# Kernel tuning notes

Hardware: AMD Instinct MI355X
Metric: run time of the kernel (lower is better)

## Reference

```python
import jax, jax.numpy as jnp
import numpy as np

ALPHA = 0.2  # LeakyReLU negative slope
NEG_INF = -9e15  # matches torch's -9e15 mask value


def gat_head(h, mask, W, a):
    # h: [N, Fin], W: [Fin, Fout], a: [2*Fout]
    # Faithful to torch GraphAttentionLayer but WITHOUT materializing the
    # N x N x 2F pairwise concat: a^T [Wh_i ; Wh_j] = (Wh_i . a1) + (Wh_j . a2).
    Wh = h @ W                                  # [N, F]
    F = W.shape[1]
    f = Wh @ a[:F]                              # [N] source term
    g = Wh @ a[F:]                              # [N] target term
    e = jax.nn.leaky_relu(f[:, None] + g[None, :], ALPHA)  # [N, N]
    e = jnp.where(mask, e, NEG_INF)
    attn = jax.nn.softmax(e, axis=1)            # row-wise softmax over neighbors
    return jax.nn.elu(attn @ Wh)                # [N, F]


def multi_head_gat(x, mask, W_heads, a_heads, W_out, a_out):
    # W_heads: [H, Fin, F], a_heads: [H, 2F]; concat heads then out-attention.
    heads = jax.vmap(gat_head, in_axes=(None, None, 0, 0))(x, mask, W_heads, a_heads)  # [H, N, F]
    N = x.shape[0]
    x = jnp.transpose(heads, (1, 0, 2)).reshape(N, -1)  # [N, H*F]
    # dropout(p=0.1) is identity in eval mode; elu applied twice as in torch code
    return jax.nn.elu(gat_head(x, mask, W_out, a_out))


def setup_inputs() -> dict:
    key = jax.random.key(0)
    ks = jax.random.split(key, 10)
    T, N, Din, H, Fh, L = 32, 512, 3, 8, 256, 3
    pose = jax.random.normal(ks[0], (T, N, Din), dtype=jnp.float32)
    adj = (jax.random.uniform(ks[1], (N, N)) < 0.06).astype(jnp.int32)
    adj = jnp.maximum(adj, jnp.eye(N, dtype=jnp.int32))
    s = 0.05  # xavier-ish scale, keeps logits stable
    return {
        "pose_sequence": pose,
        "adjacency_matrix": adj,
        "Wp": jax.random.normal(ks[2], (Din, Fh), jnp.float32) * s,
        "bp": jnp.zeros((Fh,), jnp.float32),
        "W_heads": jax.random.normal(ks[3], (L, H, Fh, Fh), jnp.float32) * s,
        "a_heads": jax.random.normal(ks[4], (L, H, 2 * Fh), jnp.float32) * s,
        "W_out": jax.random.normal(ks[5], (L, H * Fh, Fh), jnp.float32) * s,
        "a_out": jax.random.normal(ks[6], (L, 2 * Fh), jnp.float32) * s,
        "Wo": jax.random.normal(ks[7], (Fh, Fh), jnp.float32) * s,
        "bo": jnp.zeros((Fh,), jnp.float32),
    }


def reference(pose_sequence, adjacency_matrix, Wp, bp, W_heads, a_heads, W_out, a_out, Wo, bo):
    mask = adjacency_matrix > 0  # [N, N] bool
    n_layers = W_heads.shape[0]

    def frame(p):  # p: [N, Din]
        x = p @ Wp + bp  # input projection -> [N, Fh]
        for l in range(n_layers):
            x = multi_head_gat(x, mask, W_heads[l], a_heads[l], W_out[l], a_out[l])
        return x.mean(0) @ Wo + bo  # per-frame pooled output [Fh]

    return jax.vmap(frame)(pose_sequence)  # [T, Fh]
```

## Files before the change

kernel.cpp:

```cpp
#include <hip/hip_runtime.h>
#include <hip/hip_bf16.h>
#include <cstdint>
#include <cstddef>


typedef short s16x8 __attribute__((ext_vector_type(8)));
typedef float f32x4 __attribute__((ext_vector_type(4)));

__device__ __forceinline__ void async_copy16(const void* g, void* l) {
    __builtin_amdgcn_global_load_lds(
        (const __attribute__((address_space(1))) void*)g,
        (__attribute__((address_space(3))) void*)l, 16, 0, 0);
}
__device__ __forceinline__ float fast_elu(float v) {
    return v > 0.f ? v : (__expf(v) - 1.f);
}
__device__ __forceinline__ float bf2f(unsigned short u) {
    unsigned int x = (unsigned int)u << 16;
    return __uint_as_float(x);
}
__device__ __forceinline__ unsigned short f2bf(float f) {
    __hip_bfloat16 h = __float2bfloat16(f);
    return *(unsigned short*)&h;
}

__global__ __launch_bounds__(256)
void build_csr_kernel(const int* __restrict__ adj, int* __restrict__ cnt,
                      int* __restrict__ idxout)
{
    int row  = blockIdx.x * 4 + (threadIdx.x >> 6);
    int lane = threadIdx.x & 63;
    if (row >= 512) return;
    int base = 0;
    for (int j0 = 0; j0 < 512; j0 += 64) {
        int j = j0 + lane;
        bool pred = adj[row * 512 + j] > 0;
        unsigned long long m = __ballot(pred);
        if (pred) {
            int pos = __popcll(m & ((1ull << lane) - 1ull));
            idxout[row * 512 + base + pos] = j;
        }
        base += __popcll(m);
    }
    if (lane == 0) cnt[row] = base;
}

__global__ __launch_bounds__(256)
void transpose_bf16_kernel(const float* __restrict__ in,
                           __hip_bfloat16* __restrict__ ob, int K, int N)
{
    int b = blockIdx.z;
    int k0 = blockIdx.y * 32, n0 = blockIdx.x * 32;
    __shared__ float tile[32][33];
    int tx = threadIdx.x & 31, ty = threadIdx.x >> 5;
    const float* inb = in + (size_t)b * K * N;
    #pragma unroll
    for (int r = 0; r < 32; r += 8)
        tile[ty + r][tx] = inb[(size_t)(k0 + ty + r) * N + n0 + tx];
    __syncthreads();
    __hip_bfloat16* obb = ob + (size_t)b * K * N;
    #pragma unroll
    for (int r = 0; r < 32; r += 8)
        obb[(size_t)(n0 + ty + r) * K + k0 + tx] = __float2bfloat16(tile[tx][ty + r]);
}

__global__ __launch_bounds__(256)
void w12_kernel(const float* __restrict__ W, const float* __restrict__ a,
                float* __restrict__ w1, float* __restrict__ w2)
{
    int b = blockIdx.x, k = threadIdx.x;
    const float* Wb = W + (size_t)b * 256 * 256 + (size_t)k * 256;
    const float* ab = a + (size_t)b * 512;
    float s1 = 0.f, s2 = 0.f;
    for (int n = 0; n < 256; ++n) {
        float w = Wb[n];
        s1 = fmaf(w, ab[n], s1);
        s2 = fmaf(w, ab[256 + n], s2);
    }
    w1[b * 256 + k] = s1;
    w2[b * 256 + k] = s2;
}

__global__ __launch_bounds__(256)
void proj_fg_kernel(const float* __restrict__ pose, const float* __restrict__ Wp,
                    const float* __restrict__ bp,
                    const float* __restrict__ w1, const float* __restrict__ w2,
                    __hip_bfloat16* __restrict__ xB,
                    float* __restrict__ fbuf, float* __restrict__ gbuf)
{
    int w = threadIdx.x >> 6, lane = threadIdx.x & 63;
    int row = blockIdx.x * 4 + w;
    float p0 = pose[row * 3 + 0], p1 = pose[row * 3 + 1], p2 = pose[row * 3 + 2];
    int c4 = lane * 4;
    float4 w0v = *(const float4*)&Wp[0 * 256 + c4];
    float4 w1v_ = *(const float4*)&Wp[1 * 256 + c4];
    float4 w2v_ = *(const float4*)&Wp[2 * 256 + c4];
    float4 bv = *(const float4*)&bp[c4];
    float4 xv;
    xv.x = fmaf(p0, w0v.x, fmaf(p1, w1v_.x, fmaf(p2, w2v_.x, bv.x)));
    xv.y = fmaf(p0, w0v.y, fmaf(p1, w1v_.y, fmaf(p2, w2v_.y, bv.y)));
    xv.z = fmaf(p0, w0v.z, fmaf(p1, w1v_.z, fmaf(p2, w2v_.z, bv.z)));
    xv.w = fmaf(p0, w0v.w, fmaf(p1, w1v_.w, fmaf(p2, w2v_.w, bv.w)));
    ushort4 b4 = {f2bf(xv.x), f2bf(xv.y), f2bf(xv.z), f2bf(xv.w)};
    *(ushort4*)&xB[(size_t)row * 256 + c4] = b4;

    float sf[8], sg[8];
    #pragma unroll
    for (int h = 0; h < 8; ++h) {
        float4 a1 = *(const float4*)&w1[h * 256 + c4];
        float4 a2 = *(const float4*)&w2[h * 256 + c4];
        sf[h] = xv.x * a1.x + xv.y * a1.y + xv.z * a1.z + xv.w * a1.w;
        sg[h] = xv.x * a2.x + xv.y * a2.y + xv.z * a2.z + xv.w * a2.w;
    }
    #pragma unroll
    for (int off = 32; off > 0; off >>= 1)
        #pragma unroll
        for (int h = 0; h < 8; ++h) {
            sf[h] += __shfl_xor(sf[h], off);
            sg[h] += __shfl_xor(sg[h], off);
        }
    if (lane == 0) {
        float4 a = {sf[0], sf[1], sf[2], sf[3]}, b = {sf[4], sf[5], sf[6], sf[7]};
        float4 c = {sg[0], sg[1], sg[2], sg[3]}, d = {sg[4], sg[5], sg[6], sg[7]};
        *(float4*)&fbuf[(size_t)row * 8]     = a;
        *(float4*)&fbuf[(size_t)row * 8 + 4] = b;
        *(float4*)&gbuf[(size_t)row * 8]     = c;
        *(float4*)&gbuf[(size_t)row * 8 + 4] = d;
    }
}

__global__ __launch_bounds__(256)
void gemm_mfma_kernel(const __hip_bfloat16* __restrict__ A,
                      const __hip_bfloat16* __restrict__ B,
                      __hip_bfloat16* __restrict__ partB,
                      __hip_bfloat16* __restrict__ outB,
                      int M, int N, int Kld, int Klen,
                      long strideAz, long strideBz, long strideCz,
                      int outStride, int colOffZ)
{
    int z = blockIdx.z;
    const __hip_bfloat16* az = A + (size_t)z * strideAz;
    const __hip_bfloat16* bz = B + (size_t)z * strideBz;
    int m0 = blockIdx.y * 64, n0 = blockIdx.x * 128;

    __shared__ __align__(16) unsigned short lsA[2 * 64 * 32];
    __shared__ __align__(16) unsigned short lsB[2 * 128 * 32];

    int tid = threadIdx.x, w = tid >> 6, lane = tid & 63;
    int qr = w >> 1, qc = w & 1;
    int l15 = lane & 15, kgp = lane >> 4;

    f32x4 acc[2][4];
    #pragma unroll
    for (int i = 0; i < 2; i++)
        #pragma unroll
        for (int j = 0; j < 4; j++)
            acc[i][j] = (f32x4){0.f, 0.f, 0.f, 0.f};

    for (int k0 = 0; k0 < Klen; k0 += 64) {
        __syncthreads();
        #pragma unroll
        for (int cc = 0; cc < 6; ++cc) {
            int chunk = w * 6 + cc;
            if (chunk < 8) {
                int pp = chunk >> 2, lc = chunk & 3;
                int g = lc * 64 + lane;
                int row = g >> 2;
                int kg = (g & 3) ^ ((row + (row >> 2)) & 3);
                async_copy16(az + (size_t)(m0 + row) * Kld + k0 + pp * 32 + kg * 8,
                             &lsA[pp * 2048 + (size_t)g * 8]);
            } else {
                int bc = chunk - 8;
                int pp = bc >> 3, lc = bc & 7;
                int g = lc * 64 + lane;
                int row = g >> 2;
                int kg = (g & 3) ^ ((row + (row >> 2)) & 3);
                async_copy16(bz + (size_t)(n0 + row) * Kld + k0 + pp * 32 + kg * 8,
                             &lsB[pp * 4096 + (size_t)g * 8]);
            }
        }
        __syncthreads();

        #pragma unroll
        for (int pp = 0; pp < 2; ++pp) {
            s16x8 fa[2], fb[4];
            #pragma unroll
            for (int tr = 0; tr < 2; ++tr) {
                int row = qr * 32 + tr * 16 + l15;
                int cell = row * 4 + (kgp ^ ((row + (row >> 2)) & 3));
                fa[tr] = *(const s16x8*)&lsA[pp * 2048 + cell * 8];
            }
            #pragma unroll
            for (int tc = 0; tc < 4; ++tc) {
                int nn = qc * 64 + tc * 16 + l15;
                int cell = nn * 4 + (kgp ^ ((nn + (nn >> 2)) & 3));
                fb[tc] = *(const s16x8*)&lsB[pp * 4096 + cell * 8];
            }
            #pragma unroll
            for (int tr = 0; tr < 2; ++tr)
                #pragma unroll
                for (int tc = 0; tc < 4; ++tc)
                    acc[tr][tc] = __builtin_amdgcn_mfma_f32_16x16x32_bf16(
                        fa[tr], fb[tc], acc[tr][tc], 0, 0, 0);
        }
    }
    if (outB) {
        #pragma unroll
        for (int tr = 0; tr < 2; ++tr) {
            int rbase = m0 + qr * 32 + tr * 16 + (lane >> 4) * 4;
            #pragma unroll
            for (int tc = 0; tc < 4; ++tc) {
                int col = z * colOffZ + n0 + qc * 64 + tc * 16 + l15;
                #pragma unroll
                for (int r = 0; r < 4; ++r) {
                    float o = fast_elu(acc[tr][tc][r]);
                    outB[(size_t)(rbase + r) * outStride + col] = __float2bfloat16(o);
                }
            }
        }
    } else {
        __hip_bfloat16* Cz = partB + (size_t)z * strideCz;
        #pragma unroll
        for (int tr = 0; tr < 2; ++tr) {
            int rbase = m0 + qr * 32 + tr * 16 + (lane >> 4) * 4;
            #pragma unroll
            for (int tc = 0; tc < 4; ++tc) {
                int col = n0 + qc * 64 + tc * 16 + l15;
                #pragma unroll
                for (int r = 0; r < 4; ++r)
                    Cz[(size_t)(rbase + r) * N + col] = __float2bfloat16(acc[tr][tc][r]);
            }
        }
    }
}

__global__ __launch_bounds__(256)
void reduce_fg_kernel(const __hip_bfloat16* __restrict__ part, long partStride,
                      const float* __restrict__ a,
                      __hip_bfloat16* __restrict__ whoB,
                      float* __restrict__ fAll, float* __restrict__ gAll, int R)
{
    int row = blockIdx.x * 4 + (threadIdx.x >> 6);
    int lane = threadIdx.x & 63;
    const __hip_bfloat16* p0 = part + (size_t)row * 256 + lane * 4;
    ushort4 u0 = *(const ushort4*)p0;
    ushort4 u1 = *(const ushort4*)(p0 + partStride);
    float4 v = {bf2f(u0.x) + bf2f(u1.x), bf2f(u0.y) + bf2f(u1.y),
                bf2f(u0.z) + bf2f(u1.z), bf2f(u0.w) + bf2f(u1.w)};
    ushort4 b4 = {f2bf(v.x), f2bf(v.y), f2bf(v.z), f2bf(v.w)};
    *(ushort4*)&whoB[(size_t)row * 256 + lane * 4] = b4;
    float4 a1 = *(const float4*)&a[lane * 4];
    float4 a2 = *(const float4*)&a[256 + lane * 4];
    float sf = v.x * a1.x + v.y * a1.y + v.z * a1.z + v.w * a1.w;
    float sg = v.x * a2.x + v.y * a2.y + v.z * a2.z + v.w * a2.w;
    #pragma unroll
    for (int off = 32; off > 0; off >>= 1) {
        sf += __shfl_down(sf, off);
        sg += __shfl_down(sg, off);
    }
    if (lane == 0) { fAll[row] = sf; gAll[row] = sg; }
}

__global__ __launch_bounds__(256)
void attn_heads_kernel(const __hip_bfloat16* __restrict__ xB,
                       const float* __restrict__ fbuf, const float* __restrict__ gbuf,
                       const int* __restrict__ nbr_cnt, const int* __restrict__ nbr_idx,
                       __hip_bfloat16* __restrict__ yB, int R)
{
    __shared__ float plds[4][64][8];
    int t = blockIdx.y;
    int w = threadIdx.x >> 6;
    int i = blockIdx.x * 4 + w;
    int lane = threadIdx.x & 63;
    int c = nbr_cnt[i];
    int jc = c < 64 ? c : 64;
    int row = t * 512 + i;
    const __hip_bfloat16* xt = xB + (size_t)t * 512 * 256;

    float4 fA = *(const float4*)&fbuf[(size_t)row * 8];
    float4 fB = *(const float4*)&fbuf[(size_t)row * 8 + 4];

    bool ok = lane < jc;
    int id = 0;
    float4 gA = {0.f, 0.f, 0.f, 0.f}, gB = {0.f, 0.f, 0.f, 0.f};
    if (ok) {
        id = nbr_idx[i * 512 + lane];
        const float* gp = &gbuf[(size_t)(t * 512 + id) * 8];
        gA = *(const float4*)gp;
        gB = *(const float4*)(gp + 4);
    }
    float e[8];
    e[0] = fA.x + gA.x; e[1] = fA.y + gA.y; e[2] = fA.z + gA.z; e[3] = fA.w + gA.w;
    e[4] = fB.x + gB.x; e[5] = fB.y + gB.y; e[6] = fB.z + gB.z; e[7] = fB.w + gB.w;
    float p[8];
    #pragma unroll
    for (int h = 0; h < 8; ++h) {
        float eh = ok ? (e[h] >= 0.f ? e[h] : 0.2f * e[h]) : -3.0e38f;
        float pe = ok ? __expf(eh) : 0.f;
        float s = pe;
        #pragma unroll
        for (int off = 32; off > 0; off >>= 1) s += __shfl_xor(s, off);
        p[h] = pe * (1.f / s);
    }
    float4 pa = {p[0], p[1], p[2], p[3]}, pb = {p[4], p[5], p[6], p[7]};
    *(float4*)&plds[w][lane][0] = pa;
    *(float4*)&plds[w][lane][4] = pb;

    float4 acc[8];
    #pragma unroll
    for (int h = 0; h < 8; ++h) acc[h] = (float4){0.f, 0.f, 0.f, 0.f};
    int f4 = lane * 4;
    #pragma unroll 8
    for (int j = 0; j < jc; ++j) {
        int idj = __shfl(id, j);
        float4 pA = *(const float4*)&plds[w][j][0];
        float4 pB = *(const float4*)&plds[w][j][4];
        ushort4 xu = *(const ushort4*)&xt[(size_t)idj * 256 + f4];
        float4 xv = {bf2f(xu.x), bf2f(xu.y), bf2f(xu.z), bf2f(xu.w)};
        acc[0].x = fmaf(pA.x, xv.x, acc[0].x); acc[0].y = fmaf(pA.x, xv.y, acc[0].y);
        acc[0].z = fmaf(pA.x, xv.z, acc[0].z); acc[0].w = fmaf(pA.x, xv.w, acc[0].w);
        acc[1].x = fmaf(pA.y, xv.x, acc[1].x); acc[1].y = fmaf(pA.y, xv.y, acc[1].y);
        acc[1].z = fmaf(pA.y, xv.z, acc[1].z); acc[1].w = fmaf(pA.y, xv.w, acc[1].w);
        acc[2].x = fmaf(pA.z, xv.x, acc[2].x); acc[2].y = fmaf(pA.z, xv.y, acc[2].y);
        acc[2].z = fmaf(pA.z, xv.z, acc[2].z); acc[2].w = fmaf(pA.z, xv.w, acc[2].w);
        acc[3].x = fmaf(pA.w, xv.x, acc[3].x); acc[3].y = fmaf(pA.w, xv.y, acc[3].y);
        acc[3].z = fmaf(pA.w, xv.z, acc[3].z); acc[3].w = fmaf(pA.w, xv.w, acc[3].w);
        acc[4].x = fmaf(pB.x, xv.x, acc[4].x); acc[4].y = fmaf(pB.x, xv.y, acc[4].y);
        acc[4].z = fmaf(pB.x, xv.z, acc[4].z); acc[4].w = fmaf(pB.x, xv.w, acc[4].w);
        acc[5].x = fmaf(pB.y, xv.x, acc[5].x); acc[5].y = fmaf(pB.y, xv.y, acc[5].y);
        acc[5].z = fmaf(pB.y, xv.z, acc[5].z); acc[5].w = fmaf(pB.y, xv.w, acc[5].w);
        acc[6].x = fmaf(pB.z, xv.x, acc[6].x); acc[6].y = fmaf(pB.z, xv.y, acc[6].y);
        acc[6].z = fmaf(pB.z, xv.z, acc[6].z); acc[6].w = fmaf(pB.z, xv.w, acc[6].w);
        acc[7].x = fmaf(pB.w, xv.x, acc[7].x); acc[7].y = fmaf(pB.w, xv.y, acc[7].y);
        acc[7].z = fmaf(pB.w, xv.z, acc[7].z); acc[7].w = fmaf(pB.w, xv.w, acc[7].w);
    }

    #pragma unroll
    for (int h = 0; h < 8; ++h) {
        ushort4 b4 = {f2bf(acc[h].x), f2bf(acc[h].y), f2bf(acc[h].z), f2bf(acc[h].w)};
        size_t ob = (size_t)h * R * 256 + (size_t)row * 256 + f4;
        *(ushort4*)&yB[ob] = b4;
    }
}

__global__ __launch_bounds__(256)
void attn_out_kernel(const __hip_bfloat16* __restrict__ whoB,
                     const float* __restrict__ fAll, const float* __restrict__ gAll,
                     const int* __restrict__ nbr_cnt, const int* __restrict__ nbr_idx,
                     __hip_bfloat16* __restrict__ xB,
                     const float* __restrict__ w1n, const float* __restrict__ w2n,
                     float* __restrict__ fbuf, float* __restrict__ gbuf)
{
    int t = blockIdx.y;
    int i = blockIdx.x * 4 + (threadIdx.x >> 6);
    int lane = threadIdx.x & 63;
    const __hip_bfloat16* whF = whoB + (size_t)t * 512 * 256;
    int c = nbr_cnt[i];
    int jc = c < 64 ? c : 64;

    float fi = fAll[t * 512 + i];
    const float* g = gAll + t * 512;
    bool ok = lane < jc;
    int id = ok ? nbr_idx[i * 512 + lane] : 0;
    float p = 0.f;
    if (ok) {
        float ee = fi + g[id];
        float e = ee >= 0.f ? ee : 0.2f * ee;
        p = __expf(e);
    }
    float s = p;
    #pragma unroll
    for (int off = 32; off > 0; off >>= 1) s += __shfl_xor(s, off);
    p *= (1.f / s);

    float4 acc = {0.f, 0.f, 0.f, 0.f};
    int f4 = lane * 4;
    #pragma unroll 8
    for (int j = 0; j < jc; ++j) {
        float pj = __shfl(p, j);
        int  idj = __shfl(id, j);
        ushort4 vu = *(const ushort4*)&whF[(size_t)idj * 256 + f4];
        acc.x = fmaf(pj, bf2f(vu.x), acc.x);
        acc.y = fmaf(pj, bf2f(vu.y), acc.y);
        acc.z = fmaf(pj, bf2f(vu.z), acc.z);
        acc.w = fmaf(pj, bf2f(vu.w), acc.w);
    }
    float o[4] = {acc.x, acc.y, acc.z, acc.w};
    #pragma unroll
    for (int k = 0; k < 4; ++k)
        o[k] = fast_elu(fast_elu(o[k]));
    float4 ov = {o[0], o[1], o[2], o[3]};
    int row = t * 512 + i;
    ushort4 b4 = {f2bf(ov.x), f2bf(ov.y), f2bf(ov.z), f2bf(ov.w)};
    *(ushort4*)&xB[(size_t)row * 256 + f4] = b4;

    if (w1n) {
        float sf[8], sg[8];
        #pragma unroll
        for (int h = 0; h < 8; ++h) {
            float4 w1v = *(const float4*)&w1n[h * 256 + f4];
            float4 w2v = *(const float4*)&w2n[h * 256 + f4];
            sf[h] = ov.x * w1v.x + ov.y * w1v.y + ov.z * w1v.z + ov.w * w1v.w;
            sg[h] = ov.x * w2v.x + ov.y * w2v.y + ov.z * w2v.z + ov.w * w2v.w;
        }
        #pragma unroll
        for (int off = 32; off > 0; off >>= 1)
            #pragma unroll
            for (int h = 0; h < 8; ++h) {
                sf[h] += __shfl_xor(sf[h], off);
                sg[h] += __shfl_xor(sg[h], off);
            }
        if (lane == 0) {
            float4 a = {sf[0], sf[1], sf[2], sf[3]}, b = {sf[4], sf[5], sf[6], sf[7]};
            float4 cc = {sg[0], sg[1], sg[2], sg[3]}, d = {sg[4], sg[5], sg[6], sg[7]};
            *(float4*)&fbuf[(size_t)row * 8]     = a;
            *(float4*)&fbuf[(size_t)row * 8 + 4] = b;
            *(float4*)&gbuf[(size_t)row * 8]     = cc;
            *(float4*)&gbuf[(size_t)row * 8 + 4] = d;
        }
    }
}

__global__ __launch_bounds__(256)
void final_kernel(const __hip_bfloat16* __restrict__ xB, const float* __restrict__ Wo,
                  const float* __restrict__ bo, float* __restrict__ out)
{
    int t = blockIdx.x, c = threadIdx.x;
    __shared__ float pooled[256];
    float s = 0.f;
    const __hip_bfloat16* xt = xB + (size_t)t * 512 * 256;
    for (int n = 0; n < 512; ++n) s += __bfloat162float(xt[(size_t)n * 256 + c]);
    pooled[c] = s * (1.f / 512.f);
    __syncthreads();
    float o = bo[c];
    for (int k = 0; k < 256; k++) o = fmaf(pooled[k], Wo[k * 256 + c], o);
    out[t * 256 + c] = o;
}

extern "C" void kernel_launch(void* const* d_in, const int* in_sizes, int n_in,
                              void* d_out, int out_size, void* d_ws, size_t ws_size,
                              hipStream_t stream)
{
    const float* pose   = (const float*)d_in[0];
    const int*   adj    = (const int*)  d_in[1];
    const float* Wp     = (const float*)d_in[2];
    const float* bp     = (const float*)d_in[3];
    const float* Wh_w   = (const float*)d_in[4];
    const float* a_h    = (const float*)d_in[5];
    const float* W_outw = (const float*)d_in[6];
    const float* a_o    = (const float*)d_in[7];
    const float* Wo     = (const float*)d_in[8];
    const float* bo     = (const float*)d_in[9];
    float* out = (float*)d_out;

    const int T = 32, N = 512, F = 256, H = 8, L = 3, Din = 3;

    auto align256 = [](size_t b) { return (b + 255) & ~(size_t)255; };
    auto need = [&](int TC) -> size_t {
        size_t R = (size_t)TC * N;
        size_t b = 0;
        b += align256(R * F * 2);
        b += align256((size_t)H * R * F * 2);
        b += align256(R * (size_t)H * F * 2);
        b += align256(2 * R * F * 2);
        b += align256(R * F * 2);
        b += 2 * align256(R * 8 * 4);
        b += 2 * align256(R * 4);
        b += 2 * align256((size_t)L * H * F * F * 2);
        b += 2 * align256((size_t)L * H * F * 4);
        b += align256(512 * 4) + align256(512 * 512 * 4);
        return b + 4096;
    };
    int TC = 32;
    while (TC > 1 && need(TC) > ws_size) TC >>= 1;
    size_t R = (size_t)TC * N;

    char* wp = (char*)d_ws;
    auto alloc = [&](size_t bytes) -> char* {
        char* r = wp; wp += (bytes + 255) & ~(size_t)255; return r;
    };
    __hip_bfloat16* xB     = (__hip_bfloat16*)alloc(R * F * 2);
    __hip_bfloat16* yB     = (__hip_bfloat16*)alloc((size_t)H * R * F * 2);
    __hip_bfloat16* xcatB  = (__hip_bfloat16*)alloc(R * (size_t)H * F * 2);
    __hip_bfloat16* partBf = (__hip_bfloat16*)alloc(2 * R * F * 2);
    __hip_bfloat16* whoB   = (__hip_bfloat16*)alloc(R * F * 2);
    float*          fbuf   = (float*)alloc(R * 8 * 4);
    float*          gbuf   = (float*)alloc(R * 8 * 4);
    float*          fAll   = (float*)alloc(R * 4);
    float*          gAll   = (float*)alloc(R * 4);
    __hip_bfloat16* wtb    = (__hip_bfloat16*)alloc((size_t)L * H * F * F * 2);
    __hip_bfloat16* wotb   = (__hip_bfloat16*)alloc((size_t)L * H * F * F * 2);
    float*          w1     = (float*)alloc((size_t)L * H * F * 4);
    float*          w2     = (float*)alloc((size_t)L * H * F * 4);
    int*            ncnt   = (int*)alloc(512 * 4);
    int*            nidx   = (int*)alloc(512 * 512 * 4);

    build_csr_kernel<<<128, 256, 0, stream>>>(adj, ncnt, nidx);
    transpose_bf16_kernel<<<dim3(F / 32, F / 32, L * H), 256, 0, stream>>>(
        Wh_w, wtb, F, F);
    transpose_bf16_kernel<<<dim3(F / 32, (H * F) / 32, L), 256, 0, stream>>>(
        W_outw, wotb, H * F, F);
    w12_kernel<<<L * H, 256, 0, stream>>>(Wh_w, a_h, w1, w2);

    for (int t0 = 0; t0 < T; t0 += TC) {
        proj_fg_kernel<<<(unsigned)(R / 4), 256, 0, stream>>>(
            pose + (size_t)t0 * N * Din, Wp, bp, w1, w2, xB, fbuf, gbuf);

        for (int l = 0; l < L; l++) {
            attn_heads_kernel<<<dim3(128, TC), 256, 0, stream>>>(
                xB, fbuf, gbuf, ncnt, nidx, yB, (int)R);
            gemm_mfma_kernel<<<dim3(F / 128, (unsigned)(R / 64), H), 256, 0, stream>>>(
                yB, wtb + (size_t)l * H * F * F,
                nullptr, xcatB,
                (int)R, F, F, F,
                (long)R * F, (long)F * F, 0, H * F, F);
            gemm_mfma_kernel<<<dim3(F / 128, (unsigned)(R / 64), 2), 256, 0, stream>>>(
                xcatB, wotb + (size_t)l * H * F * F,
                partBf, nullptr,
                (int)R, F, H * F, H * F / 2,
                (long)(H * F / 2), (long)(H * F / 2), (long)R * F, 0, 0);
            reduce_fg_kernel<<<(unsigned)(R / 4), 256, 0, stream>>>(
                partBf, (long)R * F, a_o + (size_t)l * 2 * F, whoB, fAll, gAll, (int)R);
            const float* w1n = (l + 1 < L) ? w1 + (size_t)(l + 1) * H * F : nullptr;
            const float* w2n = (l + 1 < L) ? w2 + (size_t)(l + 1) * H * F : nullptr;
            attn_out_kernel<<<dim3(128, TC), 256, 0, stream>>>(
                whoB, fAll, gAll, ncnt, nidx, xB, w1n, w2n, fbuf, gbuf);
        }
        final_kernel<<<TC, 256, 0, stream>>>(xB, Wo, bo, out + (size_t)t0 * F);
    }
}
```

Before: 639.2 us.

## Switch storage to fp16 and use packed fdot2 pair aggregation in attention

Converts all bf16 intermediates and weights to fp16 so the GEMMs use fp16 MFMA and the attention aggregation can use v_dot2 on packed half pairs. Neighbor pairs are processed two at a time, with probabilities packed as half2 in LDS and neighbor indices read as scalars from the CSR list instead of via shuffles. The CSR builder pads indices with zeros so the odd tail pair reads a valid row with zero weight. This halves the FMA instruction count in the gather loops, at the cost of fp16 range and precision risk and fp16-rounded attention weights.

```diff
diff --git a/kernel.cpp b/kernel.cpp
--- a/kernel.cpp
+++ b/kernel.cpp
@@ -1,11 +1,13 @@
 #include <hip/hip_runtime.h>
-#include <hip/hip_bf16.h>
+#include <hip/hip_fp16.h>
 #include <cstdint>
 #include <cstddef>
 
 
-typedef short s16x8 __attribute__((ext_vector_type(8)));
+typedef _Float16 f16x2 __attribute__((ext_vector_type(2)));
+typedef _Float16 f16x8 __attribute__((ext_vector_type(8)));
 typedef float f32x4 __attribute__((ext_vector_type(4)));
+typedef unsigned int uint32;
 
 __device__ __forceinline__ void async_copy16(const void* g, void* l) {
     __builtin_amdgcn_global_load_lds(
@@ -15,13 +17,11 @@
 __device__ __forceinline__ float fast_elu(float v) {
     return v > 0.f ? v : (__expf(v) - 1.f);
 }
-__device__ __forceinline__ float bf2f(unsigned short u) {
-    unsigned int x = (unsigned int)u << 16;
-    return __uint_as_float(x);
-}
-__device__ __forceinline__ unsigned short f2bf(float f) {
-    __hip_bfloat16 h = __float2bfloat16(f);
-    return *(unsigned short*)&h;
+__device__ __forceinline__ unsigned short f2h(float f) {
+    return __builtin_bit_cast(unsigned short, (_Float16)f);
+}
+__device__ __forceinline__ float h2f(unsigned short u) {
+    return (float)__builtin_bit_cast(_Float16, u);
 }
 
 __global__ __launch_bounds__(256)
@@ -42,12 +42,14 @@
         }
         base += __popcll(m);
     }
+    int s = base + lane;
+    if (s < 64) idxout[row * 512 + s] = 0;
     if (lane == 0) cnt[row] = base;
 }
 
 __global__ __launch_bounds__(256)
-void transpose_bf16_kernel(const float* __restrict__ in,
-                           __hip_bfloat16* __restrict__ ob, int K, int N)
+void transpose_f16_kernel(const float* __restrict__ in,
+                          unsigned short* __restrict__ ob, int K, int N)
 {
     int b = blockIdx.z;
     int k0 = blockIdx.y * 32, n0 = blockIdx.x * 32;
@@ -58,10 +60,10 @@
     for (int r = 0; r < 32; r += 8)
         tile[ty + r][tx] = inb[(size_t)(k0 + ty + r) * N + n0 + tx];
     __syncthreads();
-    __hip_bfloat16* obb = ob + (size_t)b * K * N;
+    unsigned short* obb = ob + (size_t)b * K * N;
     #pragma unroll
     for (int r = 0; r < 32; r += 8)
-        obb[(size_t)(n0 + ty + r) * K + k0 + tx] = __float2bfloat16(tile[tx][ty + r]);
+        obb[(size_t)(n0 + ty + r) * K + k0 + tx] = f2h(tile[tx][ty + r]);
 }
 
 __global__ __launch_bounds__(256)
@@ -85,7 +87,7 @@
 void proj_fg_kernel(const float* __restrict__ pose, const float* __restrict__ Wp,
                     const float* __restrict__ bp,
                     const float* __restrict__ w1, const float* __restrict__ w2,
-                    __hip_bfloat16* __restrict__ xB,
+                    unsigned short* __restrict__ xH,
                     float* __restrict__ fbuf, float* __restrict__ gbuf)
 {
     int w = threadIdx.x >> 6, lane = threadIdx.x & 63;
@@ -101,8 +103,8 @@
     xv.y = fmaf(p0, w0v.y, fmaf(p1, w1v_.y, fmaf(p2, w2v_.y, bv.y)));
     xv.z = fmaf(p0, w0v.z, fmaf(p1, w1v_.z, fmaf(p2, w2v_.z, bv.z)));
     xv.w = fmaf(p0, w0v.w, fmaf(p1, w1v_.w, fmaf(p2, w2v_.w, bv.w)));
-    ushort4 b4 = {f2bf(xv.x), f2bf(xv.y), f2bf(xv.z), f2bf(xv.w)};
-    *(ushort4*)&xB[(size_t)row * 256 + c4] = b4;
+    ushort4 b4 = {f2h(xv.x), f2h(xv.y), f2h(xv.z), f2h(xv.w)};
+    *(ushort4*)&xH[(size_t)row * 256 + c4] = b4;
 
     float sf[8], sg[8];
     #pragma unroll
@@ -130,17 +132,17 @@
 }
 
 __global__ __launch_bounds__(256)
-void gemm_mfma_kernel(const __hip_bfloat16* __restrict__ A,
-                      const __hip_bfloat16* __restrict__ B,
-                      __hip_bfloat16* __restrict__ partB,
-                      __hip_bfloat16* __restrict__ outB,
+void gemm_mfma_kernel(const unsigned short* __restrict__ A,
+                      const unsigned short* __restrict__ B,
+                      unsigned short* __restrict__ partB,
+                      unsigned short* __restrict__ outB,
                       int M, int N, int Kld, int Klen,
                       long strideAz, long strideBz, long strideCz,
                       int outStride, int colOffZ)
 {
     int z = blockIdx.z;
-    const __hip_bfloat16* az = A + (size_t)z * strideAz;
-    const __hip_bfloat16* bz = B + (size_t)z * strideBz;
+    const unsigned short* az = A + (size_t)z * strideAz;
+    const unsigned short* bz = B + (size_t)z * strideBz;
     int m0 = blockIdx.y * 64, n0 = blockIdx.x * 128;
 
     __shared__ __align__(16) unsigned short lsA[2 * 64 * 32];
@@ -183,24 +185,24 @@
 
         #pragma unroll
         for (int pp = 0; pp < 2; ++pp) {
-            s16x8 fa[2], fb[4];
+            f16x8 fa[2], fb[4];
             #pragma unroll
             for (int tr = 0; tr < 2; ++tr) {
                 int row = qr * 32 + tr * 16 + l15;
                 int cell = row * 4 + (kgp ^ ((row + (row >> 2)) & 3));
-                fa[tr] = *(const s16x8*)&lsA[pp * 2048 + cell * 8];
+                fa[tr] = *(const f16x8*)&lsA[pp * 2048 + cell * 8];
             }
             #pragma unroll
             for (int tc = 0; tc < 4; ++tc) {
                 int nn = qc * 64 + tc * 16 + l15;
                 int cell = nn * 4 + (kgp ^ ((nn + (nn >> 2)) & 3));
-                fb[tc] = *(const s16x8*)&lsB[pp * 4096 + cell * 8];
+                fb[tc] = *(const f16x8*)&lsB[pp * 4096 + cell * 8];
             }
             #pragma unroll
             for (int tr = 0; tr < 2; ++tr)
                 #pragma unroll
                 for (int tc = 0; tc < 4; ++tc)
-                    acc[tr][tc] = __builtin_amdgcn_mfma_f32_16x16x32_bf16(
+                    acc[tr][tc] = __builtin_amdgcn_mfma_f32_16x16x32_f16(
                         fa[tr], fb[tc], acc[tr][tc], 0, 0, 0);
         }
     }
@@ -214,12 +216,12 @@
                 #pragma unroll
                 for (int r = 0; r < 4; ++r) {
                     float o = fast_elu(acc[tr][tc][r]);
-                    outB[(size_t)(rbase + r) * outStride + col] = __float2bfloat16(o);
+                    outB[(size_t)(rbase + r) * outStride + col] = f2h(o);
                 }
             }
         }
     } else {
-        __hip_bfloat16* Cz = partB + (size_t)z * strideCz;
+        unsigned short* Cz = partB + (size_t)z * strideCz;
         #pragma unroll
         for (int tr = 0; tr < 2; ++tr) {
             int rbase = m0 + qr * 32 + tr * 16 + (lane >> 4) * 4;
@@ -228,27 +230,27 @@
                 int col = n0 + qc * 64 + tc * 16 + l15;
                 #pragma unroll
                 for (int r = 0; r < 4; ++r)
-                    Cz[(size_t)(rbase + r) * N + col] = __float2bfloat16(acc[tr][tc][r]);
+                    Cz[(size_t)(rbase + r) * N + col] = f2h(acc[tr][tc][r]);
             }
         }
     }
 }
 
 __global__ __launch_bounds__(256)
-void reduce_fg_kernel(const __hip_bfloat16* __restrict__ part, long partStride,
+void reduce_fg_kernel(const unsigned short* __restrict__ part, long partStride,
                       const float* __restrict__ a,
-                      __hip_bfloat16* __restrict__ whoB,
+                      unsigned short* __restrict__ whoH,
                       float* __restrict__ fAll, float* __restrict__ gAll, int R)
 {
     int row = blockIdx.x * 4 + (threadIdx.x >> 6);
     int lane = threadIdx.x & 63;
-    const __hip_bfloat16* p0 = part + (size_t)row * 256 + lane * 4;
+    const unsigned short* p0 = part + (size_t)row * 256 + lane * 4;
     ushort4 u0 = *(const ushort4*)p0;
     ushort4 u1 = *(const ushort4*)(p0 + partStride);
-    float4 v = {bf2f(u0.x) + bf2f(u1.x), bf2f(u0.y) + bf2f(u1.y),
-                bf2f(u0.z) + bf2f(u1.z), bf2f(u0.w) + bf2f(u1.w)};
-    ushort4 b4 = {f2bf(v.x), f2bf(v.y), f2bf(v.z), f2bf(v.w)};
-    *(ushort4*)&whoB[(size_t)row * 256 + lane * 4] = b4;
+    float4 v = {h2f(u0.x) + h2f(u1.x), h2f(u0.y) + h2f(u1.y),
+                h2f(u0.z) + h2f(u1.z), h2f(u0.w) + h2f(u1.w)};
+    ushort4 b4 = {f2h(v.x), f2h(v.y), f2h(v.z), f2h(v.w)};
+    *(ushort4*)&whoH[(size_t)row * 256 + lane * 4] = b4;
     float4 a1 = *(const float4*)&a[lane * 4];
     float4 a2 = *(const float4*)&a[256 + lane * 4];
     float sf = v.x * a1.x + v.y * a1.y + v.z * a1.z + v.w * a1.w;
@@ -262,128 +264,150 @@
 }
 
 __global__ __launch_bounds__(256)
-void attn_heads_kernel(const __hip_bfloat16* __restrict__ xB,
+void attn_heads_kernel(const unsigned short* __restrict__ xH,
                        const float* __restrict__ fbuf, const float* __restrict__ gbuf,
                        const int* __restrict__ nbr_cnt, const int* __restrict__ nbr_idx,
-                       __hip_bfloat16* __restrict__ yB, int R)
-{
-    __shared__ float plds[4][64][8];
+                       unsigned short* __restrict__ yH, int R)
+{
+    __shared__ uint32 ppk[4][32][8];
     int t = blockIdx.y;
     int w = threadIdx.x >> 6;
     int i = blockIdx.x * 4 + w;
     int lane = threadIdx.x & 63;
-    int c = nbr_cnt[i];
-    int jc = c < 64 ? c : 64;
+    int jc = nbr_cnt[i];
+    jc = jc < 64 ? jc : 64;
     int row = t * 512 + i;
-    const __hip_bfloat16* xt = xB + (size_t)t * 512 * 256;
+    const unsigned short* xt = xH + (size_t)t * 512 * 256;
 
     float4 fA = *(const float4*)&fbuf[(size_t)row * 8];
     float4 fB = *(const float4*)&fbuf[(size_t)row * 8 + 4];
 
     bool ok = lane < jc;
-    int id = 0;
     float4 gA = {0.f, 0.f, 0.f, 0.f}, gB = {0.f, 0.f, 0.f, 0.f};
     if (ok) {
-        id = nbr_idx[i * 512 + lane];
+        int id = nbr_idx[i * 512 + lane];
         const float* gp = &gbuf[(size_t)(t * 512 + id) * 8];
         gA = *(const float4*)gp;
         gB = *(const float4*)(gp + 4);
     }
-    float e[8];
-    e[0] = fA.x + gA.x; e[1] = fA.y + gA.y; e[2] = fA.z + gA.z; e[3] = fA.w + gA.w;
-    e[4] = fB.x + gB.x; e[5] = fB.y + gB.y; e[6] = fB.z + gB.z; e[7] = fB.w + gB.w;
+    float e[8] = {fA.x + gA.x, fA.y + gA.y, fA.z + gA.z, fA.w + gA.w,
+                  fB.x + gB.x, fB.y + gB.y, fB.z + gB.z, fB.w + gB.w};
     float p[8];
     #pragma unroll
     for (int h = 0; h < 8; ++h) {
-        float eh = ok ? (e[h] >= 0.f ? e[h] : 0.2f * e[h]) : -3.0e38f;
+        float eh = e[h] >= 0.f ? e[h] : 0.2f * e[h];
         float pe = ok ? __expf(eh) : 0.f;
         float s = pe;
         #pragma unroll
         for (int off = 32; off > 0; off >>= 1) s += __shfl_xor(s, off);
         p[h] = pe * (1.f / s);
     }
-    float4 pa = {p[0], p[1], p[2], p[3]}, pb = {p[4], p[5], p[6], p[7]};
-    *(float4*)&plds[w][lane][0] = pa;
-    *(float4*)&plds[w][lane][4] = pb;
-
+    uint32 u[8];
+    #pragma unroll
+    for (int h = 0; h < 8; ++h) {
+        float pn = __shfl_xor(p[h], 1);
+        u[h] = (uint32)f2h(p[h]) | ((uint32)f2h(pn) << 16);
+    }
+    if (!(lane & 1)) {
+        int q = lane >> 1;
+        uint4 lo = {u[0], u[1], u[2], u[3]}, hi = {u[4], u[5], u[6], u[7]};
+        *(uint4*)&ppk[w][q][0] = lo;
+        *(uint4*)&ppk[w][q][4] = hi;
+    }
+
+    const int* nl = nbr_idx + (size_t)__builtin_amdgcn_readfirstlane(i) * 512;
+    int np = (jc + 1) >> 1;
     float4 acc[8];
     #pragma unroll
     for (int h = 0; h < 8; ++h) acc[h] = (float4){0.f, 0.f, 0.f, 0.f};
     int f4 = lane * 4;
-    #pragma unroll 8
-    for (int j = 0; j < jc; ++j) {
-        int idj = __shfl(id, j);
-        float4 pA = *(const float4*)&plds[w][j][0];
-        float4 pB = *(const float4*)&plds[w][j][4];
-        ushort4 xu = *(const ushort4*)&xt[(size_t)idj * 256 + f4];
-        float4 xv = {bf2f(xu.x), bf2f(xu.y), bf2f(xu.z), bf2f(xu.w)};
-        acc[0].x = fmaf(pA.x, xv.x, acc[0].x); acc[0].y = fmaf(pA.x, xv.y, acc[0].y);
-        acc[0].z = fmaf(pA.x, xv.z, acc[0].z); acc[0].w = fmaf(pA.x, xv.w, acc[0].w);
-        acc[1].x = fmaf(pA.y, xv.x, acc[1].x); acc[1].y = fmaf(pA.y, xv.y, acc[1].y);
-        acc[1].z = fmaf(pA.y, xv.z, acc[1].z); acc[1].w = fmaf(pA.y, xv.w, acc[1].w);
-        acc[2].x = fmaf(pA.z, xv.x, acc[2].x); acc[2].y = fmaf(pA.z, xv.y, acc[2].y);
-        acc[2].z = fmaf(pA.z, xv.z, acc[2].z); acc[2].w = fmaf(pA.z, xv.w, acc[2].w);
-        acc[3].x = fmaf(pA.w, xv.x, acc[3].x); acc[3].y = fmaf(pA.w, xv.y, acc[3].y);
-        acc[3].z = fmaf(pA.w, xv.z, acc[3].z); acc[3].w = fmaf(pA.w, xv.w, acc[3].w);
-        acc[4].x = fmaf(pB.x, xv.x, acc[4].x); acc[4].y = fmaf(pB.x, xv.y, acc[4].y);
-        acc[4].z = fmaf(pB.x, xv.z, acc[4].z); acc[4].w = fmaf(pB.x, xv.w, acc[4].w);
-        acc[5].x = fmaf(pB.y, xv.x, acc[5].x); acc[5].y = fmaf(pB.y, xv.y, acc[5].y);
-        acc[5].z = fmaf(pB.y, xv.z, acc[5].z); acc[5].w = fmaf(pB.y, xv.w, acc[5].w);
-        acc[6].x = fmaf(pB.z, xv.x, acc[6].x); acc[6].y = fmaf(pB.z, xv.y, acc[6].y);
-        acc[6].z = fmaf(pB.z, xv.z, acc[6].z); acc[6].w = fmaf(pB.z, xv.w, acc[6].w);
-        acc[7].x = fmaf(pB.w, xv.x, acc[7].x); acc[7].y = fmaf(pB.w, xv.y, acc[7].y);
-        acc[7].z = fmaf(pB.w, xv.z, acc[7].z); acc[7].w = fmaf(pB.w, xv.w, acc[7].w);
+    #pragma unroll 4
+    for (int q = 0; q < np; ++q) {
+        int ia = nl[2 * q], ib = nl[2 * q + 1];
+        uint4 plo = *(const uint4*)&ppk[w][q][0];
+        uint4 phi = *(const uint4*)&ppk[w][q][4];
+        uint2 xa = *(const uint2*)&xt[(size_t)ia * 256 + f4];
+        uint2 xb = *(const uint2*)&xt[(size_t)ib * 256 + f4];
+        uint32 pr0 = __builtin_amdgcn_perm(xb.x, xa.x, 0x05040100u);
+        uint32 pr1 = __builtin_amdgcn_perm(xb.x, xa.x, 0x07060302u);
+        uint32 pr2 = __builtin_amdgcn_perm(xb.y, xa.y, 0x05040100u);
+        uint32 pr3 = __builtin_amdgcn_perm(xb.y, xa.y, 0x07060302u);
+        f16x2 c0 = __builtin_bit_cast(f16x2, pr0);
+        f16x2 c1 = __builtin_bit_cast(f16x2, pr1);
+        f16x2 c2 = __builtin_bit_cast(f16x2, pr2);
+        f16x2 c3 = __builtin_bit_cast(f16x2, pr3);
+        uint32 pw[8] = {plo.x, plo.y, plo.z, plo.w, phi.x, phi.y, phi.z, phi.w};
+        #pragma unroll
+        for (int h = 0; h < 8; ++h) {
+            f16x2 ph = __builtin_bit_cast(f16x2, pw[h]);
+            acc[h].x = __builtin_amdgcn_fdot2(c0, ph, acc[h].x, false);
+            acc[h].y = __builtin_amdgcn_fdot2(c1, ph, acc[h].y, false);
+            acc[h].z = __builtin_amdgcn_fdot2(c2, ph, acc[h].z, false);
+            acc[h].w = __builtin_amdgcn_fdot2(c3, ph, acc[h].w, false);
+        }
     }
 
     #pragma unroll
     for (int h = 0; h < 8; ++h) {
-        ushort4 b4 = {f2bf(acc[h].x), f2bf(acc[h].y), f2bf(acc[h].z), f2bf(acc[h].w)};
+        ushort4 b4 = {f2h(acc[h].x), f2h(acc[h].y), f2h(acc[h].z), f2h(acc[h].w)};
         size_t ob = (size_t)h * R * 256 + (size_t)row * 256 + f4;
-        *(ushort4*)&yB[ob] = b4;
-    }
-}
-
-__global__ __launch_bounds__(256)
-void attn_out_kernel(const __hip_bfloat16* __restrict__ whoB,
+        *(ushort4*)&yH[ob] = b4;
+    }
+}
+
+__global__ __launch_bounds__(256)
+void attn_out_kernel(const unsigned short* __restrict__ whoH,
                      const float* __restrict__ fAll, const float* __restrict__ gAll,
                      const int* __restrict__ nbr_cnt, const int* __restrict__ nbr_idx,
-                     __hip_bfloat16* __restrict__ xB,
+                     unsigned short* __restrict__ xH,
                      const float* __restrict__ w1n, const float* __restrict__ w2n,
                      float* __restrict__ fbuf, float* __restrict__ gbuf)
 {
+    __shared__ uint32 pp2[4][32];
     int t = blockIdx.y;
-    int i = blockIdx.x * 4 + (threadIdx.x >> 6);
+    int w = threadIdx.x >> 6;
+    int i = blockIdx.x * 4 + w;
     int lane = threadIdx.x & 63;
-    const __hip_bfloat16* whF = whoB + (size_t)t * 512 * 256;
-    int c = nbr_cnt[i];
-    int jc = c < 64 ? c : 64;
+    const unsigned short* whF = whoH + (size_t)t * 512 * 256;
+    int jc = nbr_cnt[i];
+    jc = jc < 64 ? jc : 64;
 
     float fi = fAll[t * 512 + i];
     const float* g = gAll + t * 512;
     bool ok = lane < jc;
-    int id = ok ? nbr_idx[i * 512 + lane] : 0;
     float p = 0.f;
     if (ok) {
+        int id = nbr_idx[i * 512 + lane];
         float ee = fi + g[id];
-        float e = ee >= 0.f ? ee : 0.2f * ee;
-        p = __expf(e);
+        float e2 = ee >= 0.f ? ee : 0.2f * ee;
+        p = __expf(e2);
     }
     float s = p;
     #pragma unroll
     for (int off = 32; off > 0; off >>= 1) s += __shfl_xor(s, off);
     p *= (1.f / s);
-
+    float pn = __shfl_xor(p, 1);
+    if (!(lane & 1))
+        pp2[w][lane >> 1] = (uint32)f2h(p) | ((uint32)f2h(pn) << 16);
+
+    const int* nl = nbr_idx + (size_t)__builtin_amdgcn_readfirstlane(i) * 512;
+    int np = (jc + 1) >> 1;
     float4 acc = {0.f, 0.f, 0.f, 0.f};
     int f4 = lane * 4;
-    #pragma unroll 8
-    for (int j = 0; j < jc; ++j) {
-        float pj = __shfl(p, j);
-        int  idj = __shfl(id, j);
-        ushort4 vu = *(const ushort4*)&whF[(size_t)idj * 256 + f4];
-        acc.x = fmaf(pj, bf2f(vu.x), acc.x);
-        acc.y = fmaf(pj, bf2f(vu.y), acc.y);
-        acc.z = fmaf(pj, bf2f(vu.z), acc.z);
-        acc.w = fmaf(pj, bf2f(vu.w), acc.w);
+    #pragma unroll 4
+    for (int q = 0; q < np; ++q) {
+        int ia = nl[2 * q], ib = nl[2 * q + 1];
+        f16x2 ph = __builtin_bit_cast(f16x2, pp2[w][q]);
+        uint2 xa = *(const uint2*)&whF[(size_t)ia * 256 + f4];
+        uint2 xb = *(const uint2*)&whF[(size_t)ib * 256 + f4];
+        uint32 pr0 = __builtin_amdgcn_perm(xb.x, xa.x, 0x05040100u);
+        uint32 pr1 = __builtin_amdgcn_perm(xb.x, xa.x, 0x07060302u);
+        uint32 pr2 = __builtin_amdgcn_perm(xb.y, xa.y, 0x05040100u);
+        uint32 pr3 = __builtin_amdgcn_perm(xb.y, xa.y, 0x07060302u);
+        acc.x = __builtin_amdgcn_fdot2(__builtin_bit_cast(f16x2, pr0), ph, acc.x, false);
+        acc.y = __builtin_amdgcn_fdot2(__builtin_bit_cast(f16x2, pr1), ph, acc.y, false);
+        acc.z = __builtin_amdgcn_fdot2(__builtin_bit_cast(f16x2, pr2), ph, acc.z, false);
+        acc.w = __builtin_amdgcn_fdot2(__builtin_bit_cast(f16x2, pr3), ph, acc.w, false);
     }
     float o[4] = {acc.x, acc.y, acc.z, acc.w};
     #pragma unroll
@@ -391,8 +415,8 @@
         o[k] = fast_elu(fast_elu(o[k]));
     float4 ov = {o[0], o[1], o[2], o[3]};
     int row = t * 512 + i;
-    ushort4 b4 = {f2bf(ov.x), f2bf(ov.y), f2bf(ov.z), f2bf(ov.w)};
-    *(ushort4*)&xB[(size_t)row * 256 + f4] = b4;
+    ushort4 b4 = {f2h(ov.x), f2h(ov.y), f2h(ov.z), f2h(ov.w)};
+    *(ushort4*)&xH[(size_t)row * 256 + f4] = b4;
 
     if (w1n) {
         float sf[8], sg[8];
@@ -422,14 +446,14 @@
 }
 
 __global__ __launch_bounds__(256)
-void final_kernel(const __hip_bfloat16* __restrict__ xB, const float* __restrict__ Wo,
+void final_kernel(const unsigned short* __restrict__ xH, const float* __restrict__ Wo,
                   const float* __restrict__ bo, float* __restrict__ out)
 {
     int t = blockIdx.x, c = threadIdx.x;
     __shared__ float pooled[256];
     float s = 0.f;
-    const __hip_bfloat16* xt = xB + (size_t)t * 512 * 256;
-    for (int n = 0; n < 512; ++n) s += __bfloat162float(xt[(size_t)n * 256 + c]);
+    const unsigned short* xt = xH + (size_t)t * 512 * 256;
+    for (int n = 0; n < 512; ++n) s += h2f(xt[(size_t)n * 256 + c]);
     pooled[c] = s * (1.f / 512.f);
     __syncthreads();
     float o = bo[c];
@@ -479,26 +503,26 @@
     auto alloc = [&](size_t bytes) -> char* {
         char* r = wp; wp += (bytes + 255) & ~(size_t)255; return r;
     };
-    __hip_bfloat16* xB     = (__hip_bfloat16*)alloc(R * F * 2);
-    __hip_bfloat16* yB     = (__hip_bfloat16*)alloc((size_t)H * R * F * 2);
-    __hip_bfloat16* xcatB  = (__hip_bfloat16*)alloc(R * (size_t)H * F * 2);
-    __hip_bfloat16* partBf = (__hip_bfloat16*)alloc(2 * R * F * 2);
-    __hip_bfloat16* whoB   = (__hip_bfloat16*)alloc(R * F * 2);
+    unsigned short* xB     = (unsigned short*)alloc(R * F * 2);
+    unsigned short* yB     = (unsigned short*)alloc((size_t)H * R * F * 2);
+    unsigned short* xcatB  = (unsigned short*)alloc(R * (size_t)H * F * 2);
+    unsigned short* partBf = (unsigned short*)alloc(2 * R * F * 2);
+    unsigned short* whoB   = (unsigned short*)alloc(R * F * 2);
     float*          fbuf   = (float*)alloc(R * 8 * 4);
     float*          gbuf   = (float*)alloc(R * 8 * 4);
     float*          fAll   = (float*)alloc(R * 4);
     float*          gAll   = (float*)alloc(R * 4);
-    __hip_bfloat16* wtb    = (__hip_bfloat16*)alloc((size_t)L * H * F * F * 2);
-    __hip_bfloat16* wotb   = (__hip_bfloat16*)alloc((size_t)L * H * F * F * 2);
+    unsigned short* wtb    = (unsigned short*)alloc((size_t)L * H * F * F * 2);
+    unsigned short* wotb   = (unsigned short*)alloc((size_t)L * H * F * F * 2);
     float*          w1     = (float*)alloc((size_t)L * H * F * 4);
     float*          w2     = (float*)alloc((size_t)L * H * F * 4);
     int*            ncnt   = (int*)alloc(512 * 4);
     int*            nidx   = (int*)alloc(512 * 512 * 4);
 
     build_csr_kernel<<<128, 256, 0, stream>>>(adj, ncnt, nidx);
-    transpose_bf16_kernel<<<dim3(F / 32, F / 32, L * H), 256, 0, stream>>>(
+    transpose_f16_kernel<<<dim3(F / 32, F / 32, L * H), 256, 0, stream>>>(
         Wh_w, wtb, F, F);
-    transpose_bf16_kernel<<<dim3(F / 32, (H * F) / 32, L), 256, 0, stream>>>(
+    transpose_f16_kernel<<<dim3(F / 32, (H * F) / 32, L), 256, 0, stream>>>(
         W_outw, wotb, H * F, F);
     w12_kernel<<<L * H, 256, 0, stream>>>(Wh_w, a_h, w1, w2);
 
```

New measurement: 574.8 us. 1.11x faster.
